# Kernel optimization log

Measured on AMD Instinct MI355X. Metric: run time of the kernel, lower is better.

The kernel has to match this reference:

```python
import jax, jax.numpy as jnp
import numpy as np

L, EMB, NH, HD, V = 4, 1024, 16, 64, 16000
Q, B, M = 512, 4, 512


def layer_norm(x, g, b, eps=1e-5):
    mu = jnp.mean(x, -1, keepdims=True)
    var = jnp.mean((x - mu) ** 2, -1, keepdims=True)
    return (x - mu) * jax.lax.rsqrt(var + eps) * g + b


def rel_shift(x):
    # x: [q, i, b, h] -> Transformer-XL relative shift via zero-pad + reshape
    q, i, bb, h = x.shape
    zp = jnp.zeros((q, 1, bb, h), x.dtype)
    return jnp.concatenate([zp, x], axis=1).reshape(i + 1, q, bb, h)[1:].reshape(q, i, bb, h)


def setup_inputs() -> dict:
    key = jax.random.key(0)
    ks = jax.random.split(key, 12)
    s = 0.02
    return {
        'input_idxs': jax.random.randint(ks[0], (Q, B), 0, V, dtype=jnp.int32),
        'memory': jax.random.normal(ks[1], (L, M, B, EMB), jnp.float32),
        'embedding': jax.random.normal(ks[2], (V, EMB), jnp.float32) * s,
        'proj_b': jnp.zeros((V,), jnp.float32),
        'u_bias': jax.random.normal(ks[3], (NH, HD), jnp.float32) * s,
        'v_bias': jax.random.normal(ks[4], (NH, HD), jnp.float32) * s,
        'Wq': jax.random.normal(ks[5], (L, NH * HD, EMB), jnp.float32) * s,
        'Wkv': jax.random.normal(ks[6], (L, 2 * NH * HD, EMB), jnp.float32) * s,
        'Wp': jax.random.normal(ks[7], (L, NH * HD, EMB), jnp.float32) * s,
        'fc_w': jax.random.normal(ks[8], (L, EMB, NH * HD), jnp.float32) * s,
        'ff1_w': jax.random.normal(ks[9], (L, 4 * EMB, EMB), jnp.float32) * s,
        'ff1_b': jnp.zeros((L, 4 * EMB), jnp.float32),
        'ff2_w': jax.random.normal(ks[10], (L, EMB, 4 * EMB), jnp.float32) * s,
        'ff2_b': jnp.zeros((L, EMB), jnp.float32),
        'ln_g': jnp.ones((L, EMB), jnp.float32),
        'ln_b': jnp.zeros((L, EMB), jnp.float32),
    }


def reference(input_idxs, memory, embedding, proj_b, u_bias, v_bias, Wq, Wkv, Wp,
              fc_w, ff1_w, ff1_b, ff2_w, ff2_b, ln_g, ln_b):
    # NOTE: faithful to the source, which uses scale = 1 / head_dim**5 (not **0.5)
    scale = 1.0 / (HD ** 5)
    x = embedding[input_idxs] * jnp.asarray(EMB ** 0.5, jnp.float32)  # [Q,B,E]

    # sinusoidal relative positions, descending M+Q-1 .. 0
    pos = jnp.arange(M + Q - 1, -1, -1, dtype=jnp.float32)
    inv_freq = 1.0 / (10000.0 ** (jnp.arange(0, EMB, 2, dtype=jnp.float32) / EMB))
    angle = pos[:, None] * inv_freq[None, :]
    emb_pos = jnp.concatenate([jnp.sin(angle), jnp.cos(angle)], axis=1)  # [M+Q,E]

    mask = jnp.triu(jnp.ones((Q, M + Q), bool), k=1 + M)  # [Q,I]

    for l in range(L):
        e = jnp.concatenate([memory[l], x], axis=0)  # [I,B,E], I = M+Q
        kv = jnp.einsum('ibe,fe->ibf', e, Wkv[l])
        k, v = jnp.split(kv, 2, axis=-1)
        k = k.reshape(M + Q, B, NH, HD)
        v = v.reshape(M + Q, B, NH, HD)
        q = jnp.einsum('qbe,fe->qbf', x, Wq[l]).reshape(Q, B, NH, HD)
        p = (emb_pos @ Wp[l].T).reshape(M + Q, NH, HD)

        att_c = jnp.einsum('qbhd,ibhd->qibh', q + u_bias, k)
        att_p = rel_shift(jnp.einsum('qbhd,ihd->qibh', q + v_bias, p))
        att = att_c + att_p
        att = jnp.where(mask[:, :, None, None], -jnp.inf, att)
        att = jax.nn.softmax(att * scale, axis=1)

        o = jnp.einsum('qibh,ibhd->qbhd', att, v).reshape(Q, B, NH * HD)
        o = o @ fc_w[l].T
        h = layer_norm(o + x, ln_g[l], ln_b[l])
        f = jax.nn.relu(h @ ff1_w[l].T + ff1_b[l]) @ ff2_w[l].T + ff2_b[l]
        x = layer_norm(f + h, ln_g[l], ln_b[l])

    return x @ embedding.T + proj_b  # tied projection, [Q,B,V]
```

## Files before the change

### kernel.cpp

```cpp
#include <hip/hip_runtime.h>


typedef unsigned short u16;
typedef unsigned int u32;
typedef __bf16 bf16x8 __attribute__((ext_vector_type(8)));
typedef float f32x4 __attribute__((ext_vector_type(4)));

#define AS1 __attribute__((address_space(1)))
#define AS3 __attribute__((address_space(3)))

__device__ __forceinline__ u16 f2bf(float f) {
  u32 u = __float_as_uint(f);
  u32 r = (u + 0x7FFFu + ((u >> 16) & 1u)) >> 16;
  return (u16)r;
}
__device__ __forceinline__ float bf2f(u16 u) {
  return __uint_as_float(((u32)u) << 16);
}

struct alignas(8) us4 { u16 x, y, z, w; };

__global__ void k_conv(const float* __restrict__ src, u16* __restrict__ dst, int n4) {
  int i = blockIdx.x * blockDim.x + threadIdx.x;
  int stride = gridDim.x * blockDim.x;
  const float4* s4 = (const float4*)src;
  us4* d4 = (us4*)dst;
  for (; i < n4; i += stride) {
    float4 v = s4[i];
    us4 o; o.x = f2bf(v.x); o.y = f2bf(v.y); o.z = f2bf(v.z); o.w = f2bf(v.w);
    d4[i] = o;
  }
}

__global__ void k_conv5(const float* __restrict__ s0, u16* __restrict__ d0,
                        const float* __restrict__ s1, u16* __restrict__ d1,
                        const float* __restrict__ s2, u16* __restrict__ d2,
                        const float* __restrict__ s3, u16* __restrict__ d3,
                        const float* __restrict__ s4, u16* __restrict__ d4) {
  const int n0 = 262144, n1 = 262144, n2 = 1048576, n3 = 1048576;
  const int total = 3145728;
  int i = blockIdx.x * 256 + threadIdx.x;
  int stride = gridDim.x * 256;
  for (; i < total; i += stride) {
    const float* s; u16* d; int j = i;
    if (j < n0) { s = s0; d = d0; }
    else if ((j -= n0) < n1) { s = s1; d = d1; }
    else if ((j -= n1) < n2) { s = s2; d = d2; }
    else if ((j -= n2) < n3) { s = s3; d = d3; }
    else { j -= n3; s = s4; d = d4; }
    float4 v = ((const float4*)s)[j];
    us4 o; o.x = f2bf(v.x); o.y = f2bf(v.y); o.z = f2bf(v.z); o.w = f2bf(v.w);
    ((us4*)d)[j] = o;
  }
}

__global__ void k_embed(const int* __restrict__ idx, const float* __restrict__ emb,
                        float* __restrict__ x, u16* __restrict__ xb) {
  int r = blockIdx.x, t = threadIdx.x;
  int id = idx[r];
  float4 v = ((const float4*)(emb + (size_t)id * 1024))[t];
  v.x *= 32.0f; v.y *= 32.0f; v.z *= 32.0f; v.w *= 32.0f;
  ((float4*)(x + (size_t)r * 1024))[t] = v;
  us4 o; o.x = f2bf(v.x); o.y = f2bf(v.y); o.z = f2bf(v.z); o.w = f2bf(v.w);
  ((us4*)(xb + (size_t)r * 1024))[t] = o;
}

__global__ void k_ln(const float* __restrict__ a, const float* __restrict__ res,
                     const float* __restrict__ g, const float* __restrict__ bb,
                     float* __restrict__ outf, u16* __restrict__ outb) {
  int r = blockIdx.x, t = threadIdx.x;
  float4 va = ((const float4*)(a + (size_t)r * 1024))[t];
  float4 vr = ((const float4*)(res + (size_t)r * 1024))[t];
  float y0 = va.x + vr.x, y1 = va.y + vr.y, y2 = va.z + vr.z, y3 = va.w + vr.w;
  float s = y0 + y1 + y2 + y3;
  float sq = y0 * y0 + y1 * y1 + y2 * y2 + y3 * y3;
  for (int o = 32; o > 0; o >>= 1) { s += __shfl_xor(s, o); sq += __shfl_xor(sq, o); }
  __shared__ float ls[8];
  int w = t >> 6;
  if ((t & 63) == 0) { ls[w * 2] = s; ls[w * 2 + 1] = sq; }
  __syncthreads();
  s = ls[0] + ls[2] + ls[4] + ls[6];
  sq = ls[1] + ls[3] + ls[5] + ls[7];
  float mu = s * (1.0f / 1024.0f);
  float var = sq * (1.0f / 1024.0f) - mu * mu;
  float rs = rsqrtf(var + 1e-5f);
  float4 vg = ((const float4*)g)[t];
  float4 vb = ((const float4*)bb)[t];
  float o0 = (y0 - mu) * rs * vg.x + vb.x;
  float o1 = (y1 - mu) * rs * vg.y + vb.y;
  float o2v = (y2 - mu) * rs * vg.z + vb.z;
  float o3 = (y3 - mu) * rs * vg.w + vb.w;
  float4 of; of.x = o0; of.y = o1; of.z = o2v; of.w = o3;
  ((float4*)(outf + (size_t)r * 1024))[t] = of;
  us4 oo; oo.x = f2bf(o0); oo.y = f2bf(o1); oo.z = f2bf(o2v); oo.w = f2bf(o3);
  ((us4*)(outb + (size_t)r * 1024))[t] = oo;
}

__global__ void k_psum(const u16* __restrict__ v, float* __restrict__ part) {
  int bx = blockIdx.x;
  int c = bx >> 2, b = bx & 3;
  int f4 = threadIdx.x;
  float4 s = {0.f, 0.f, 0.f, 0.f};
  for (int j = 0; j < 64; j++) {
    int i = c * 64 + j;
    us4 u = ((const us4*)(v + (size_t)(i * 4 + b) * 1024))[f4];
    s.x += bf2f(u.x); s.y += bf2f(u.y); s.z += bf2f(u.z); s.w += bf2f(u.w);
  }
  ((float4*)(part + (size_t)(c * 4 + b) * 1024))[f4] = s;
}

__global__ void k_pmean(const u16* __restrict__ v, const float* __restrict__ part,
                        u16* __restrict__ ob) {
  int bx = blockIdx.x;
  int qc = bx >> 2, b = bx & 3;
  int f4 = threadIdx.x;
  float4 run = {0.f, 0.f, 0.f, 0.f};
  int cend = 8 + qc;
  for (int cc = 0; cc < cend; cc++) {
    float4 p = ((const float4*)(part + (size_t)(cc * 4 + b) * 1024))[f4];
    run.x += p.x; run.y += p.y; run.z += p.z; run.w += p.w;
  }
  for (int j = 0; j < 64; j++) {
    int i = 512 + qc * 64 + j;
    us4 u = ((const us4*)(v + (size_t)(i * 4 + b) * 1024))[f4];
    run.x += bf2f(u.x); run.y += bf2f(u.y); run.z += bf2f(u.z); run.w += bf2f(u.w);
    float inv = 1.0f / (float)(i + 1);
    us4 o; o.x = f2bf(run.x * inv); o.y = f2bf(run.y * inv);
    o.z = f2bf(run.z * inv); o.w = f2bf(run.w * inv);
    ((us4*)(ob + (size_t)((i - 512) * 4 + b) * 1024))[f4] = o;
  }
}

template <int BM, int BIAS, int RELU, int OUTBF>
__global__ __launch_bounds__(256, 2) void k_gemm(
    const u16* __restrict__ A, const u16* __restrict__ A2, int split,
    const u16* __restrict__ B, float* __restrict__ Cf, u16* __restrict__ Cb,
    const float* __restrict__ bias, int M, int N, int K) {
  constexpr int SA = BM / 32;
  constexpr int NI = (BM == 128) ? 4 : 2;
  __shared__ __align__(16) u16 As[BM * 64];
  __shared__ __align__(16) u16 Bs[128 * 64];
  const int tid = threadIdx.x;
  const int lane = tid & 63, wid = tid >> 6;
  const int la = lane & 15, lb = lane >> 4;
  int bx = blockIdx.x, by = blockIdx.y;
  {
    int gx = gridDim.x;
    int nwg = gx * gridDim.y;
    int orig = by * gx + bx;
    int q = nwg >> 3, r = nwg & 7;
    int xcd = orig & 7, j = orig >> 3;
    int wg = (xcd < r ? xcd * (q + 1) : r * (q + 1) + (xcd - r) * q) + j;
    bx = wg % gx; by = wg / gx;
  }
  const int row0 = bx * BM, col0 = by * 128;
  const int wm = (BM == 128) ? (wid >> 1) : 0;
  const int wn = (BM == 128) ? (wid & 1) : wid;
  const int mbase = wm * 64;
  const int nbase = (BM == 128) ? wn * 64 : wn * 32;
  const size_t Kb = (size_t)K * 2;
  const u16* Au = A; int arow = row0;
  if (row0 >= split) { Au = A2; arow = row0 - split; }
  const char* Ab = (const char*)Au + (size_t)arow * Kb;
  const char* Bb = (const char*)B + (size_t)col0 * Kb;
  f32x4 acc[4][NI] = {};
  for (int k0 = 0; k0 < K; k0 += 64) {
#pragma unroll
    for (int s = 0; s < SA; s++) {
      int off = s * 4096 + tid * 16;
      int rr = off >> 7, cb = off & 127;
      __builtin_amdgcn_global_load_lds(
          (AS1 void*)(Ab + (size_t)rr * Kb + (size_t)(k0 * 2 + cb)),
          (AS3 void*)((char*)As + s * 4096 + wid * 1024), 16, 0, 0);
    }
#pragma unroll
    for (int s = 0; s < 4; s++) {
      int off = s * 4096 + tid * 16;
      int rr = off >> 7, cb = off & 127;
      __builtin_amdgcn_global_load_lds(
          (AS1 void*)(Bb + (size_t)rr * Kb + (size_t)(k0 * 2 + cb)),
          (AS3 void*)((char*)Bs + s * 4096 + wid * 1024), 16, 0, 0);
    }
    __syncthreads();
    bf16x8 af[2][4], bfv[2][NI];
#pragma unroll
    for (int kk = 0; kk < 2; kk++) {
#pragma unroll
      for (int i = 0; i < 4; i++)
        af[kk][i] = *reinterpret_cast<const bf16x8*>(
            &As[(mbase + i * 16 + la) * 64 + kk * 32 + lb * 8]);
#pragma unroll
      for (int i = 0; i < NI; i++)
        bfv[kk][i] = *reinterpret_cast<const bf16x8*>(
            &Bs[(nbase + i * 16 + la) * 64 + kk * 32 + lb * 8]);
    }
#pragma unroll
    for (int kk = 0; kk < 2; kk++)
#pragma unroll
      for (int mi = 0; mi < 4; mi++)
#pragma unroll
        for (int ni = 0; ni < NI; ni++)
          acc[mi][ni] = __builtin_amdgcn_mfma_f32_16x16x32_bf16(
              af[kk][mi], bfv[kk][ni], acc[mi][ni], 0, 0, 0);
    __syncthreads();
  }
#pragma unroll
  for (int ni = 0; ni < NI; ni++) {
    int c = col0 + nbase + ni * 16 + la;
    float bv = 0.f;
    if (BIAS) bv = bias[c];
#pragma unroll
    for (int mi = 0; mi < 4; mi++) {
#pragma unroll
      for (int j = 0; j < 4; j++) {
        int rr = row0 + mbase + mi * 16 + lb * 4 + j;
        float vv = acc[mi][ni][j];
        if (BIAS) vv += bv;
        if (RELU) vv = fmaxf(vv, 0.f);
        if (OUTBF) Cb[(size_t)rr * N + c] = f2bf(vv);
        else       Cf[(size_t)rr * N + c] = vv;
      }
    }
  }
}

extern "C" void kernel_launch(void* const* d_in, const int* in_sizes, int n_in,
                              void* d_out, int out_size, void* d_ws, size_t ws_size,
                              hipStream_t stream) {
  const int* idxs = (const int*)d_in[0];
  const float* memory = (const float*)d_in[1];
  const float* embedding = (const float*)d_in[2];
  const float* proj_b = (const float*)d_in[3];
  const float* Wkv = (const float*)d_in[7];
  const float* fc_w = (const float*)d_in[9];
  const float* ff1_w = (const float*)d_in[10];
  const float* ff1_b = (const float*)d_in[11];
  const float* ff2_w = (const float*)d_in[12];
  const float* ff2_b = (const float*)d_in[13];
  const float* ln_g = (const float*)d_in[14];
  const float* ln_b = (const float*)d_in[15];
  float* out = (float*)d_out;

  float* ws = (float*)d_ws;
  float* x    = ws + 0;
  float* h    = ws + 2097152;
  float* o2   = ws + 4194304;
  u16* xb     = (u16*)(ws + 6291456);
  u16* hb     = (u16*)(ws + 7340032);
  u16* ob     = (u16*)(ws + 8388608);
  float* part = ws + 9437184;
  u16* wvv    = (u16*)(ws + 9502720);
  u16* wfc    = (u16*)(ws + 10027008);
  u16* wf1    = (u16*)(ws + 10551296);
  u16* wf2    = (u16*)(ws + 12648448);
  float* big  = ws + 14745600;
  u16* vbuf   = (u16*)(big);
  u16* memb   = (u16*)(big + 2097152);
  u16* f1     = (u16*)(big + 3145728);
  u16* embb   = (u16*)(big);

  const int BIG = 1 << 30;
  k_embed<<<2048, 256, 0, stream>>>(idxs, embedding, x, xb);

  for (int l = 0; l < 4; l++) {
    k_conv5<<<2048, 256, 0, stream>>>(
        Wkv + (size_t)l * 2097152 + 1048576, wvv,
        fc_w + (size_t)l * 1048576, wfc,
        ff1_w + (size_t)l * 4194304, wf1,
        ff2_w + (size_t)l * 4194304, wf2,
        memory + (size_t)l * 2097152, memb);

    k_gemm<64, 0, 0, 1><<<dim3(64, 8), 256, 0, stream>>>(
        memb, xb, 2048, wvv, nullptr, vbuf, nullptr, 4096, 1024, 1024);

    k_psum<<<64, 256, 0, stream>>>(vbuf, part);
    k_pmean<<<32, 256, 0, stream>>>(vbuf, part, ob);

    k_gemm<64, 0, 0, 0><<<dim3(32, 8), 256, 0, stream>>>(
        ob, ob, BIG, wfc, o2, nullptr, nullptr, 2048, 1024, 1024);
    k_ln<<<2048, 256, 0, stream>>>(o2, x, ln_g + l * 1024, ln_b + l * 1024, h, hb);
    k_gemm<128, 1, 1, 1><<<dim3(16, 32), 256, 0, stream>>>(
        hb, hb, BIG, wf1, nullptr, f1, ff1_b + l * 4096, 2048, 4096, 1024);
    k_gemm<64, 1, 0, 0><<<dim3(32, 8), 256, 0, stream>>>(
        f1, f1, BIG, wf2, o2, nullptr, ff2_b + l * 1024, 2048, 1024, 4096);
    k_ln<<<2048, 256, 0, stream>>>(o2, h, ln_g + l * 1024, ln_b + l * 1024, x, xb);
  }

  {
    int n4 = 16384000 >> 2;
    k_conv<<<4096, 256, 0, stream>>>(embedding, embb, n4);
  }
  k_gemm<128, 1, 0, 0><<<dim3(16, 125), 256, 0, stream>>>(
      xb, xb, BIG, embb, out, nullptr, proj_b, 2048, 16000, 1024);
}
```

Before: 1.130 ms.

## Double-buffer GEMM LDS loads, split-K small GEMMs, finer prefix-mean chunks

```diff
diff --git a/kernel.cpp b/kernel.cpp
--- a/kernel.cpp
+++ b/kernel.cpp
@@ -65,13 +65,19 @@
   ((us4*)(xb + (size_t)r * 1024))[t] = o;
 }
 
-__global__ void k_ln(const float* __restrict__ a, const float* __restrict__ res,
+template <int TWO>
+__global__ void k_ln(const float* __restrict__ a0, const float* __restrict__ a1,
+                     const float* __restrict__ res,
                      const float* __restrict__ g, const float* __restrict__ bb,
                      float* __restrict__ outf, u16* __restrict__ outb) {
   int r = blockIdx.x, t = threadIdx.x;
-  float4 va = ((const float4*)(a + (size_t)r * 1024))[t];
+  float4 va = ((const float4*)(a0 + (size_t)r * 1024))[t];
   float4 vr = ((const float4*)(res + (size_t)r * 1024))[t];
   float y0 = va.x + vr.x, y1 = va.y + vr.y, y2 = va.z + vr.z, y3 = va.w + vr.w;
+  if (TWO) {
+    float4 v1 = ((const float4*)(a1 + (size_t)r * 1024))[t];
+    y0 += v1.x; y1 += v1.y; y2 += v1.z; y3 += v1.w;
+  }
   float s = y0 + y1 + y2 + y3;
   float sq = y0 * y0 + y1 * y1 + y2 * y2 + y3 * y3;
   for (int o = 32; o > 0; o >>= 1) { s += __shfl_xor(s, o); sq += __shfl_xor(sq, o); }
@@ -101,8 +107,8 @@
   int c = bx >> 2, b = bx & 3;
   int f4 = threadIdx.x;
   float4 s = {0.f, 0.f, 0.f, 0.f};
-  for (int j = 0; j < 64; j++) {
-    int i = c * 64 + j;
+  for (int j = 0; j < 16; j++) {
+    int i = c * 16 + j;
     us4 u = ((const us4*)(v + (size_t)(i * 4 + b) * 1024))[f4];
     s.x += bf2f(u.x); s.y += bf2f(u.y); s.z += bf2f(u.z); s.w += bf2f(u.w);
   }
@@ -115,13 +121,13 @@
   int qc = bx >> 2, b = bx & 3;
   int f4 = threadIdx.x;
   float4 run = {0.f, 0.f, 0.f, 0.f};
-  int cend = 8 + qc;
+  int cend = 32 + qc;
   for (int cc = 0; cc < cend; cc++) {
     float4 p = ((const float4*)(part + (size_t)(cc * 4 + b) * 1024))[f4];
     run.x += p.x; run.y += p.y; run.z += p.z; run.w += p.w;
   }
-  for (int j = 0; j < 64; j++) {
-    int i = 512 + qc * 64 + j;
+  for (int j = 0; j < 16; j++) {
+    int i = 512 + qc * 16 + j;
     us4 u = ((const us4*)(v + (size_t)(i * 4 + b) * 1024))[f4];
     run.x += bf2f(u.x); run.y += bf2f(u.y); run.z += bf2f(u.z); run.w += bf2f(u.w);
     float inv = 1.0f / (float)(i + 1);
@@ -134,12 +140,13 @@
 template <int BM, int BIAS, int RELU, int OUTBF>
 __global__ __launch_bounds__(256, 2) void k_gemm(
     const u16* __restrict__ A, const u16* __restrict__ A2, int split,
-    const u16* __restrict__ B, float* __restrict__ Cf, u16* __restrict__ Cb,
-    const float* __restrict__ bias, int M, int N, int K) {
+    const u16* __restrict__ B, float* __restrict__ Cf, float* __restrict__ CfB,
+    u16* __restrict__ Cb, const float* __restrict__ bias,
+    int M, int N, int Ksub, int ldK) {
   constexpr int SA = BM / 32;
   constexpr int NI = (BM == 128) ? 4 : 2;
-  __shared__ __align__(16) u16 As[BM * 64];
-  __shared__ __align__(16) u16 Bs[128 * 64];
+  __shared__ __align__(16) u16 As[2][BM * 64];
+  __shared__ __align__(16) u16 Bs[2][128 * 64];
   const int tid = threadIdx.x;
   const int lane = tid & 63, wid = tid >> 6;
   const int la = lane & 15, lb = lane >> 4;
@@ -158,20 +165,21 @@
   const int wn = (BM == 128) ? (wid & 1) : wid;
   const int mbase = wm * 64;
   const int nbase = (BM == 128) ? wn * 64 : wn * 32;
-  const size_t Kb = (size_t)K * 2;
+  const size_t Kb = (size_t)ldK * 2;
   const u16* Au = A; int arow = row0;
   if (row0 >= split) { Au = A2; arow = row0 - split; }
-  const char* Ab = (const char*)Au + (size_t)arow * Kb;
-  const char* Bb = (const char*)B + (size_t)col0 * Kb;
-  f32x4 acc[4][NI] = {};
-  for (int k0 = 0; k0 < K; k0 += 64) {
+  const size_t kzoff = (size_t)blockIdx.z * Ksub * 2;
+  const char* Ab = (const char*)Au + (size_t)arow * Kb + kzoff;
+  const char* Bb = (const char*)B + (size_t)col0 * Kb + kzoff;
+
+  auto STAGE = [&](int bf, int k0) {
 #pragma unroll
     for (int s = 0; s < SA; s++) {
       int off = s * 4096 + tid * 16;
       int rr = off >> 7, cb = off & 127;
       __builtin_amdgcn_global_load_lds(
           (AS1 void*)(Ab + (size_t)rr * Kb + (size_t)(k0 * 2 + cb)),
-          (AS3 void*)((char*)As + s * 4096 + wid * 1024), 16, 0, 0);
+          (AS3 void*)((char*)&As[bf][0] + s * 4096 + wid * 1024), 16, 0, 0);
     }
 #pragma unroll
     for (int s = 0; s < 4; s++) {
@@ -179,20 +187,37 @@
       int rr = off >> 7, cb = off & 127;
       __builtin_amdgcn_global_load_lds(
           (AS1 void*)(Bb + (size_t)rr * Kb + (size_t)(k0 * 2 + cb)),
-          (AS3 void*)((char*)Bs + s * 4096 + wid * 1024), 16, 0, 0);
-    }
-    __syncthreads();
+          (AS3 void*)((char*)&Bs[bf][0] + s * 4096 + wid * 1024), 16, 0, 0);
+    }
+  };
+
+  f32x4 acc[4][NI] = {};
+  const int NT = Ksub >> 6;
+  STAGE(0, 0);
+  for (int t = 0; t < NT; t++) {
+    const int p = t & 1;
+    if (t + 1 < NT) {
+      STAGE(p ^ 1, (t + 1) << 6);
+      if (BM == 128) asm volatile("s_waitcnt vmcnt(8)" ::: "memory");
+      else           asm volatile("s_waitcnt vmcnt(6)" ::: "memory");
+    } else {
+      asm volatile("s_waitcnt vmcnt(0)" ::: "memory");
+    }
+    __builtin_amdgcn_s_barrier();
+    __builtin_amdgcn_sched_barrier(0);
+    const u16* Asp = &As[p][0];
+    const u16* Bsp = &Bs[p][0];
     bf16x8 af[2][4], bfv[2][NI];
 #pragma unroll
     for (int kk = 0; kk < 2; kk++) {
 #pragma unroll
       for (int i = 0; i < 4; i++)
         af[kk][i] = *reinterpret_cast<const bf16x8*>(
-            &As[(mbase + i * 16 + la) * 64 + kk * 32 + lb * 8]);
+            &Asp[(mbase + i * 16 + la) * 64 + kk * 32 + lb * 8]);
 #pragma unroll
       for (int i = 0; i < NI; i++)
         bfv[kk][i] = *reinterpret_cast<const bf16x8*>(
-            &Bs[(nbase + i * 16 + la) * 64 + kk * 32 + lb * 8]);
+            &Bsp[(nbase + i * 16 + la) * 64 + kk * 32 + lb * 8]);
     }
 #pragma unroll
     for (int kk = 0; kk < 2; kk++)
@@ -202,13 +227,17 @@
         for (int ni = 0; ni < NI; ni++)
           acc[mi][ni] = __builtin_amdgcn_mfma_f32_16x16x32_bf16(
               af[kk][mi], bfv[kk][ni], acc[mi][ni], 0, 0, 0);
-    __syncthreads();
-  }
+    __builtin_amdgcn_sched_barrier(0);
+    __builtin_amdgcn_s_barrier();
+    __builtin_amdgcn_sched_barrier(0);
+  }
+  float* Cout = (blockIdx.z == 1) ? CfB : Cf;
+  const int addb = BIAS && (blockIdx.z == 0);
 #pragma unroll
   for (int ni = 0; ni < NI; ni++) {
     int c = col0 + nbase + ni * 16 + la;
     float bv = 0.f;
-    if (BIAS) bv = bias[c];
+    if (BIAS) bv = addb ? bias[c] : 0.f;
 #pragma unroll
     for (int mi = 0; mi < 4; mi++) {
 #pragma unroll
@@ -218,7 +247,7 @@
         if (BIAS) vv += bv;
         if (RELU) vv = fmaxf(vv, 0.f);
         if (OUTBF) Cb[(size_t)rr * N + c] = f2bf(vv);
-        else       Cf[(size_t)rr * N + c] = vv;
+        else       Cout[(size_t)rr * N + c] = vv;
       }
     }
   }
@@ -248,7 +277,6 @@
   u16* xb     = (u16*)(ws + 6291456);
   u16* hb     = (u16*)(ws + 7340032);
   u16* ob     = (u16*)(ws + 8388608);
-  float* part = ws + 9437184;
   u16* wvv    = (u16*)(ws + 9502720);
   u16* wfc    = (u16*)(ws + 10027008);
   u16* wf1    = (u16*)(ws + 10551296);
@@ -257,7 +285,10 @@
   u16* vbuf   = (u16*)(big);
   u16* memb   = (u16*)(big + 2097152);
   u16* f1     = (u16*)(big + 3145728);
+  float* part = big + 7340032;
   u16* embb   = (u16*)(big);
+  float* fcP1 = (float*)f1;
+  float* ffP1 = (float*)vbuf;
 
   const int BIG = 1 << 30;
   k_embed<<<2048, 256, 0, stream>>>(idxs, embedding, x, xb);
@@ -270,26 +301,26 @@
         ff2_w + (size_t)l * 4194304, wf2,
         memory + (size_t)l * 2097152, memb);
 
-    k_gemm<64, 0, 0, 1><<<dim3(64, 8), 256, 0, stream>>>(
-        memb, xb, 2048, wvv, nullptr, vbuf, nullptr, 4096, 1024, 1024);
-
-    k_psum<<<64, 256, 0, stream>>>(vbuf, part);
-    k_pmean<<<32, 256, 0, stream>>>(vbuf, part, ob);
-
-    k_gemm<64, 0, 0, 0><<<dim3(32, 8), 256, 0, stream>>>(
-        ob, ob, BIG, wfc, o2, nullptr, nullptr, 2048, 1024, 1024);
-    k_ln<<<2048, 256, 0, stream>>>(o2, x, ln_g + l * 1024, ln_b + l * 1024, h, hb);
-    k_gemm<128, 1, 1, 1><<<dim3(16, 32), 256, 0, stream>>>(
-        hb, hb, BIG, wf1, nullptr, f1, ff1_b + l * 4096, 2048, 4096, 1024);
-    k_gemm<64, 1, 0, 0><<<dim3(32, 8), 256, 0, stream>>>(
-        f1, f1, BIG, wf2, o2, nullptr, ff2_b + l * 1024, 2048, 1024, 4096);
-    k_ln<<<2048, 256, 0, stream>>>(o2, h, ln_g + l * 1024, ln_b + l * 1024, x, xb);
+    k_gemm<64, 0, 0, 1><<<dim3(64, 8, 1), 256, 0, stream>>>(
+        memb, xb, 2048, wvv, nullptr, nullptr, vbuf, nullptr, 4096, 1024, 1024, 1024);
+
+    k_psum<<<256, 256, 0, stream>>>(vbuf, part);
+    k_pmean<<<128, 256, 0, stream>>>(vbuf, part, ob);
+
+    k_gemm<64, 0, 0, 0><<<dim3(32, 8, 2), 256, 0, stream>>>(
+        ob, ob, BIG, wfc, o2, fcP1, nullptr, nullptr, 2048, 1024, 512, 1024);
+    k_ln<1><<<2048, 256, 0, stream>>>(o2, fcP1, x, ln_g + l * 1024, ln_b + l * 1024, h, hb);
+    k_gemm<128, 1, 1, 1><<<dim3(16, 32, 1), 256, 0, stream>>>(
+        hb, hb, BIG, wf1, nullptr, nullptr, f1, ff1_b + l * 4096, 2048, 4096, 1024, 1024);
+    k_gemm<64, 1, 0, 0><<<dim3(32, 8, 2), 256, 0, stream>>>(
+        f1, f1, BIG, wf2, o2, ffP1, nullptr, ff2_b + l * 1024, 2048, 1024, 2048, 4096);
+    k_ln<1><<<2048, 256, 0, stream>>>(o2, ffP1, h, ln_g + l * 1024, ln_b + l * 1024, x, xb);
   }
 
   {
     int n4 = 16384000 >> 2;
     k_conv<<<4096, 256, 0, stream>>>(embedding, embb, n4);
   }
-  k_gemm<128, 1, 0, 0><<<dim3(16, 125), 256, 0, stream>>>(
-      xb, xb, BIG, embb, out, nullptr, proj_b, 2048, 16000, 1024);
-}
+  k_gemm<128, 1, 0, 0><<<dim3(16, 125, 1), 256, 0, stream>>>(
+      xb, xb, BIG, embb, out, nullptr, nullptr, proj_b, 2048, 16000, 1024, 1024);
+}
```

Result: faster. 1.039 ms (-8.0%).
